# Kernel optimization log

Measured on AMD Instinct MI355X. Metric: run time of the kernel, lower is better.

Reference implementation:

```python
import jax, jax.numpy as jnp
import numpy as np

FA, FB_CAT, FM, HID = 133, 147, 8, 100  # atom feat, bond feat (concat), mol feat, hidden
N_ATOMS, N_BONDS, N_MOLS, MAX_NB = 250000, 500000, 10000, 6
DEPTH = 3


def setup_inputs() -> dict:
    key = jax.random.key(0)
    ks = jax.random.split(key, 10)
    f_atoms = jax.random.normal(ks[0], (N_ATOMS, FA), jnp.float32)
    f_bonds = jax.random.normal(ks[1], (N_BONDS, FB_CAT), jnp.float32)
    f_mol = jax.random.normal(ks[2], (N_MOLS, FM), jnp.float32)
    a2b = jax.random.randint(ks[3], (N_ATOMS, MAX_NB), 0, N_BONDS, jnp.int32)
    b2a = jax.random.randint(ks[4], (N_BONDS,), 0, N_ATOMS, jnp.int32)
    b2revb = jax.random.randint(ks[5], (N_BONDS,), 0, N_BONDS, jnp.int32)
    # contiguous molecules of 25 atoms each -> equivalent of ascope segments
    mol_id = (jnp.arange(N_ATOMS, dtype=jnp.int32) // (N_ATOMS // N_MOLS))
    # parameters (Linear with bias=False): stored as (in, out)
    W_i = jax.random.normal(ks[6], (FB_CAT, HID), jnp.float32) * 0.05
    W_h = jax.random.normal(ks[7], (HID, HID), jnp.float32) * 0.05
    W_o = jax.random.normal(ks[8], (HID + FA, HID), jnp.float32) * 0.05
    return {"f_atoms": f_atoms, "f_bonds": f_bonds, "f_mol": f_mol,
            "W_i": W_i, "W_h": W_h, "W_o": W_o,
            "a2b": a2b, "b2a": b2a, "b2revb": b2revb,
            "mol_id": mol_id, "n_mols": N_MOLS}


def reference(f_atoms, f_bonds, f_mol, W_i, W_h, W_o, a2b, b2a, b2revb, mol_id, n_mols):
    act = jax.nn.relu
    inp = act(f_bonds @ W_i)              # (B, H)
    message = inp
    for _ in range(DEPTH - 1):
        nei = message[a2b]                # (A, MAX_NB, H) gather
        a_message = nei.sum(axis=1)       # (A, H)
        message = a_message[b2a] - message[b2revb]  # (B, H)
        message = act(inp + message @ W_h)
        # dropout p=0 (eval) -> identity
    # readout to atoms
    a_message = message[a2b].sum(axis=1)  # (A, H)
    a_input = jnp.concatenate([f_atoms, a_message], axis=1)  # (A, FA+H)
    atom_hiddens = act(a_input @ W_o)     # (A, H)
    # per-molecule mean over ragged segments (ascope equivalent)
    mol_sum = jax.ops.segment_sum(atom_hiddens, mol_id, num_segments=n_mols)
    counts = jax.ops.segment_sum(jnp.ones((atom_hiddens.shape[0],), atom_hiddens.dtype),
                                 mol_id, num_segments=n_mols)
    mol_vecs = mol_sum / jnp.maximum(counts, 1.0)[:, None]  # zero-vec for empty mols
    mol_vecs = jnp.concatenate([mol_vecs, f_mol], axis=1)   # (M, H+FM)
    return mol_vecs, atom_hiddens
```

## Files before the change

### kernel.cpp

```cpp
#include <hip/hip_runtime.h>

#define THREADS 256
#define MS 128

typedef __bf16 bf16x8 __attribute__((ext_vector_type(8)));
typedef float f32x4 __attribute__((ext_vector_type(4)));
typedef float f32x4u __attribute__((ext_vector_type(4), aligned(4)));

__device__ __forceinline__ unsigned short f2b(float x) {
    unsigned int u = __float_as_uint(x);
    u = (u + 0x7FFFu + ((u >> 16) & 1u)) >> 16;
    return (unsigned short)u;
}
__device__ __forceinline__ float b2f(unsigned short h) {
    return __uint_as_float(((unsigned int)h) << 16);
}
__device__ __forceinline__ bf16x8 as_bf(uint4 q) {
    union { uint4 q; bf16x8 v; } u; u.q = q; return u.v;
}

__device__ __forceinline__ void pack_body(const float* __restrict__ W,
                                          unsigned short* __restrict__ out,
                                          int K, int bid, int l)
{
    int kc = bid / 7, nt = bid - kc * 7;
    int k0 = kc * 32 + (l >> 4) * 8;
    int n = nt * 16 + (l & 15);
    unsigned short v[8];
    #pragma unroll
    for (int j = 0; j < 8; ++j) {
        int k = k0 + j;
        float x = (k < K && n < 100) ? W[(size_t)k * 100 + n] : 0.f;
        v[j] = f2b(x);
    }
    *(uint4*)&out[((size_t)bid * 64 + l) * 8] = *(uint4*)v;
}

__device__ __forceinline__ void pack_wo_body(const float* __restrict__ W,
                                             unsigned short* __restrict__ out,
                                             int bid, int l)
{
    int kc = bid / 7, nt = bid - kc * 7;
    int k0 = kc * 32 + (l >> 4) * 8;
    int n = nt * 16 + (l & 15);
    unsigned short v[8];
    #pragma unroll
    for (int j = 0; j < 8; ++j) {
        int k = k0 + j;
        float x = 0.f;
        if (n < 100) {
            if (k < 100)                  x = W[(size_t)(133 + k) * 100 + n];
            else if (k >= 112 && k < 245) x = W[(size_t)(k - 112) * 100 + n];
        }
        v[j] = f2b(x);
    }
    *(uint4*)&out[((size_t)bid * 64 + l) * 8] = *(uint4*)v;
}

__global__ __launch_bounds__(64) void prep(
    const float* __restrict__ Wi, const float* __restrict__ Wh, const float* __restrict__ Wo,
    unsigned short* __restrict__ wfi, unsigned short* __restrict__ wfh,
    unsigned short* __restrict__ wfo, float* __restrict__ out_mol, int nmol_floats)
{
    int bid = blockIdx.x;
    int l = threadIdx.x;
    if (bid < 35) {
        pack_body(Wi, wfi, 147, bid, l);
    } else if (bid < 63) {
        pack_body(Wh, wfh, 100, bid - 35, l);
    } else if (bid < 119) {
        pack_wo_body(Wo, wfo, bid - 63, l);
    } else {
        int idx = (bid - 119) * 64 + l;
        int stride = (gridDim.x - 119) * 64;
        for (int i = idx; i * 4 < nmol_floats; i += stride)
            *(f32x4*)&out_mol[(size_t)i * 4] = (f32x4){0.f, 0.f, 0.f, 0.f};
    }
}

__global__ __launch_bounds__(THREADS) void gather_sum_bf16(
    const unsigned short* __restrict__ msg, const int* __restrict__ a2b,
    unsigned short* __restrict__ amsg, int A)
{
    int t = blockIdx.x * THREADS + threadIdx.x;
    if (t >= A * 16) return;
    int a = t >> 4;
    int c = t & 15;
    if (c >= 14) {
        *(uint4*)&amsg[(size_t)a * MS + c * 8] = make_uint4(0u, 0u, 0u, 0u);
        return;
    }
    const int* nb = a2b + (size_t)a * 6;
    float s[8];
    #pragma unroll
    for (int e = 0; e < 8; ++e) s[e] = 0.f;
    #pragma unroll
    for (int j = 0; j < 6; ++j) {
        uint4 v = *(const uint4*)&msg[(size_t)nb[j] * MS + c * 8];
        const unsigned short* pv = (const unsigned short*)&v;
        #pragma unroll
        for (int e = 0; e < 8; ++e) s[e] += b2f(pv[e]);
    }
    unsigned short r[8];
    #pragma unroll
    for (int e = 0; e < 8; ++e) r[e] = f2b(s[e]);
    *(uint4*)&amsg[(size_t)a * MS + c * 8] = *(uint4*)r;
}

__global__ __launch_bounds__(THREADS, 2) void gemm_in(
    const float* __restrict__ fb, const unsigned short* __restrict__ wf,
    unsigned short* __restrict__ Y, int M)
{
    constexpr int KS = 168;
    __shared__ char smem[64 * KS * 2];
    unsigned short* Xs = (unsigned short*)smem;
    unsigned short* Os = (unsigned short*)smem;

    const int tid = threadIdx.x;
    const int l = tid & 63, w = tid >> 6;
    const int quad = l >> 4, c15 = l & 15;
    const int row0 = blockIdx.x * 64;

    for (int t = tid; t < 64 * 20; t += THREADS) {
        int rl = t / 20, c = t - rl * 20;
        int rr = min(row0 + rl, M - 1);
        const float* rowp = fb + (size_t)rr * 147 + c * 8;
        unsigned short tt[8];
        if (c < 18) {
            f32x4u x0 = *(const f32x4u*)(rowp);
            f32x4u x1 = *(const f32x4u*)(rowp + 4);
            #pragma unroll
            for (int e = 0; e < 4; ++e) { tt[e] = f2b(x0[e]); tt[4 + e] = f2b(x1[e]); }
        } else if (c == 18) {
            #pragma unroll
            for (int j = 0; j < 8; ++j)
                tt[j] = (j < 3) ? f2b(rowp[j]) : (unsigned short)0;
        } else {
            #pragma unroll
            for (int j = 0; j < 8; ++j) tt[j] = 0;
        }
        *(uint4*)&Xs[(size_t)rl * KS + c * 8] = *(uint4*)tt;
    }
    __syncthreads();

    f32x4 acc[7];
    #pragma unroll
    for (int nt = 0; nt < 7; ++nt) acc[nt] = (f32x4){0.f, 0.f, 0.f, 0.f};
    const unsigned short* xrow = Xs + (size_t)(w * 16 + c15) * KS + quad * 8;
    #pragma unroll
    for (int kc = 0; kc < 5; ++kc) {
        bf16x8 av = *(const bf16x8*)(xrow + kc * 32);
        #pragma unroll
        for (int nt = 0; nt < 7; ++nt) {
            uint4 bq = *(const uint4*)&wf[((size_t)(kc * 7 + nt) * 64 + l) * 8];
            acc[nt] = __builtin_amdgcn_mfma_f32_16x16x32_bf16(av, as_bf(bq), acc[nt], 0, 0, 0);
        }
    }
    __syncthreads();

    #pragma unroll
    for (int nt = 0; nt < 7; ++nt)
        #pragma unroll
        for (int reg = 0; reg < 4; ++reg)
            Os[(w * 16 + quad * 4 + reg) * 136 + nt * 16 + c15] = f2b(fmaxf(acc[nt][reg], 0.f));
    __syncthreads();

    for (int t = tid; t < 64 * 16; t += THREADS) {
        int rl = t >> 4, c = t & 15;
        int rr = row0 + rl;
        if (rr < M) {
            uint4 o = (c < 14) ? *(const uint4*)&Os[rl * 136 + c * 8]
                               : make_uint4(0u, 0u, 0u, 0u);
            *(uint4*)&Y[(size_t)rr * MS + c * 8] = o;
        }
    }
}

__global__ __launch_bounds__(THREADS, 2) void gemm_msg(
    const unsigned short* __restrict__ amsg, const unsigned short* __restrict__ msg,
    const int* __restrict__ b2a, const int* __restrict__ b2revb,
    const unsigned short* __restrict__ wf, const unsigned short* __restrict__ bias,
    unsigned short* __restrict__ Y, int M, int last)
{
    __shared__ unsigned short Os[64 * 136];
    const int tid = threadIdx.x;
    const int l = tid & 63, w = tid >> 6;
    const int quad = l >> 4, c15 = l & 15;
    const int row0 = blockIdx.x * 64;
    const int rc = min(row0 + w * 16 + c15, M - 1);
    const int iA = b2a[rc], iB = b2revb[rc];
    const unsigned short* pa = amsg + (size_t)iA * MS + quad * 8;
    const unsigned short* pb = msg  + (size_t)iB * MS + quad * 8;

    uint4 a1[4], a2[4];
    #pragma unroll
    for (int kc = 0; kc < 4; ++kc) {
        a1[kc] = *(const uint4*)(pa + kc * 32);
        a2[kc] = *(const uint4*)(pb + kc * 32);
    }

    f32x4 acc1[7], acc2[7];
    #pragma unroll
    for (int nt = 0; nt < 7; ++nt) {
        acc1[nt] = (f32x4){0.f, 0.f, 0.f, 0.f};
        acc2[nt] = (f32x4){0.f, 0.f, 0.f, 0.f};
    }
    #pragma unroll
    for (int kc = 0; kc < 4; ++kc) {
        #pragma unroll
        for (int nt = 0; nt < 7; ++nt) {
            uint4 bq = *(const uint4*)&wf[((size_t)(kc * 7 + nt) * 64 + l) * 8];
            acc1[nt] = __builtin_amdgcn_mfma_f32_16x16x32_bf16(as_bf(a1[kc]), as_bf(bq), acc1[nt], 0, 0, 0);
            acc2[nt] = __builtin_amdgcn_mfma_f32_16x16x32_bf16(as_bf(a2[kc]), as_bf(bq), acc2[nt], 0, 0, 0);
        }
    }

    #pragma unroll
    for (int nt = 0; nt < 7; ++nt)
        #pragma unroll
        for (int reg = 0; reg < 4; ++reg)
            Os[(w * 16 + quad * 4 + reg) * 136 + nt * 16 + c15] = f2b(acc1[nt][reg] - acc2[nt][reg]);
    __syncthreads();

    for (int t = tid; t < 64 * 16; t += THREADS) {
        int rl = t >> 4, c = t & 15;
        int rr = row0 + rl;
        if (rr >= M) continue;
        if (c < 14) {
            uint4 o = *(const uint4*)&Os[rl * 136 + c * 8];
            uint4 bq = *(const uint4*)&bias[(size_t)rr * MS + c * 8];
            const unsigned short* po = (const unsigned short*)&o;
            const unsigned short* pq = (const unsigned short*)&bq;
            unsigned short res[8];
            #pragma unroll
            for (int e = 0; e < 8; ++e)
                res[e] = f2b(fmaxf(b2f(po[e]) + b2f(pq[e]), 0.f));
            *(uint4*)&Y[(size_t)rr * MS + c * 8] = *(uint4*)res;
        } else if (!last) {
            *(uint4*)&Y[(size_t)rr * MS + c * 8] = make_uint4(0u, 0u, 0u, 0u);
        }
    }
}

__global__ __launch_bounds__(THREADS, 2) void gemm_out(
    const float* __restrict__ fa, const unsigned short* __restrict__ msg,
    const int* __restrict__ a2b, const unsigned short* __restrict__ wf,
    const int* __restrict__ mol_id, float* __restrict__ Y,
    float* __restrict__ out_mol, int M)
{
    constexpr int XSS = 136;
    __shared__ char smem[64 * 100 * 4];
    __shared__ int mids[64];
    unsigned short* Xs = (unsigned short*)smem;
    float* Os = (float*)smem;

    const int tid = threadIdx.x;
    const int l = tid & 63, w = tid >> 6;
    const int quad = l >> 4, c15 = l & 15;
    const int row0 = blockIdx.x * 64;

    if (tid < 64) {
        int rr = row0 + tid;
        mids[tid] = (rr < M) ? mol_id[rr] : -1;
    }

    uint4 af[5];
    {
        const int r = w * 16 + c15;
        const int rr = min(row0 + r, M - 1);
        const float* fap = fa + (size_t)rr * 133;
        #pragma unroll
        for (int kk = 0; kk < 5; ++kk) {
            int col0 = (kk + 3) * 32 + quad * 8 - 112;
            unsigned short tt[8];
            if (col0 >= 0 && col0 + 7 < 133) {
                f32x4u x0 = *(const f32x4u*)(fap + col0);
                f32x4u x1 = *(const f32x4u*)(fap + col0 + 4);
                #pragma unroll
                for (int e = 0; e < 4; ++e) { tt[e] = f2b(x0[e]); tt[4 + e] = f2b(x1[e]); }
            } else {
                #pragma unroll
                for (int j = 0; j < 8; ++j) {
                    int cc = col0 + j;
                    tt[j] = (cc >= 0 && cc < 133) ? f2b(fap[cc]) : (unsigned short)0;
                }
            }
            af[kk] = *(uint4*)tt;
        }
    }

    for (int t = tid; t < 64 * 16; t += THREADS) {
        int rl = t >> 4, c = t & 15;
        int rr = min(row0 + rl, M - 1);
        uint4 o = make_uint4(0u, 0u, 0u, 0u);
        if (c < 14) {
            const int* nb = a2b + (size_t)rr * 6;
            float s[8];
            #pragma unroll
            for (int e = 0; e < 8; ++e) s[e] = 0.f;
            #pragma unroll
            for (int j = 0; j < 6; ++j) {
                uint4 v = *(const uint4*)&msg[(size_t)nb[j] * MS + c * 8];
                const unsigned short* pv = (const unsigned short*)&v;
                #pragma unroll
                for (int e = 0; e < 8; ++e) s[e] += b2f(pv[e]);
            }
            unsigned short r8[8];
            #pragma unroll
            for (int e = 0; e < 8; ++e) r8[e] = f2b(s[e]);
            o = *(uint4*)r8;
        }
        *(uint4*)&Xs[rl * XSS + c * 8] = o;
    }
    __syncthreads();

    f32x4 acc[7];
    #pragma unroll
    for (int nt = 0; nt < 7; ++nt) acc[nt] = (f32x4){0.f, 0.f, 0.f, 0.f};
    const unsigned short* xrow = Xs + (size_t)(w * 16 + c15) * XSS + quad * 8;
    #pragma unroll
    for (int kc = 0; kc < 8; ++kc) {
        bf16x8 av;
        if (kc < 3)       av = *(const bf16x8*)(xrow + kc * 32);
        else if (kc == 3) av = (quad < 2) ? *(const bf16x8*)(xrow + 3 * 32)
                                          : as_bf(af[0]);
        else              av = as_bf(af[kc - 3]);
        #pragma unroll
        for (int nt = 0; nt < 7; ++nt) {
            uint4 bq = *(const uint4*)&wf[((size_t)(kc * 7 + nt) * 64 + l) * 8];
            acc[nt] = __builtin_amdgcn_mfma_f32_16x16x32_bf16(av, as_bf(bq), acc[nt], 0, 0, 0);
        }
    }
    __syncthreads();

    #pragma unroll
    for (int nt = 0; nt < 7; ++nt) {
        int n = nt * 16 + c15;
        if (n < 100) {
            #pragma unroll
            for (int reg = 0; reg < 4; ++reg)
                Os[(w * 16 + quad * 4 + reg) * 100 + n] = fmaxf(acc[nt][reg], 0.f);
        }
    }
    __syncthreads();

    for (int t = tid; t < 64 * 25; t += THREADS) {
        int rl = t / 25, c = t - rl * 25;
        int rr = row0 + rl;
        if (rr < M)
            *(f32x4*)&Y[(size_t)rr * 100 + c * 4] = *(const f32x4*)&Os[rl * 100 + c * 4];
    }

    if (tid < 100) {
        int c = tid;
        float s = 0.f;
        int cur = mids[0];
        #pragma unroll 1
        for (int rl = 0; rl < 64; ++rl) {
            int mid = mids[rl];
            if (mid != cur) {
                if (cur >= 0) atomicAdd(&out_mol[(size_t)cur * 108 + c], s);
                s = 0.f;
                cur = mid;
            }
            if (mid < 0) break;
            s += Os[rl * 100 + c];
        }
        if (cur >= 0) atomicAdd(&out_mol[(size_t)cur * 108 + c], s);
    }
}

__global__ __launch_bounds__(128) void finalize(
    float* __restrict__ out_mol, const float* __restrict__ f_mol,
    const int* __restrict__ mol_id, int n_atoms)
{
    int m = blockIdx.x;
    int lo = 0, hi = n_atoms;
    while (lo < hi) { int mid = (lo + hi) >> 1; if (mol_id[mid] < m) lo = mid + 1; else hi = mid; }
    int lo2 = lo, hi2 = n_atoms;
    while (lo2 < hi2) { int mid = (lo2 + hi2) >> 1; if (mol_id[mid] < m + 1) lo2 = mid + 1; else hi2 = mid; }
    float inv = 1.0f / fmaxf((float)(lo2 - lo), 1.0f);
    int c = threadIdx.x;
    if (c < 100) {
        out_mol[(size_t)m * 108 + c] *= inv;
    } else if (c < 108) {
        out_mol[(size_t)m * 108 + c] = f_mol[(size_t)m * 8 + (c - 100)];
    }
}

extern "C" void kernel_launch(void* const* d_in, const int* in_sizes, int n_in,
                              void* d_out, int out_size, void* d_ws, size_t ws_size,
                              hipStream_t stream)
{
    const float* f_atoms = (const float*)d_in[0];
    const float* f_bonds = (const float*)d_in[1];
    const float* f_mol   = (const float*)d_in[2];
    const float* W_i     = (const float*)d_in[3];
    const float* W_h     = (const float*)d_in[4];
    const float* W_o     = (const float*)d_in[5];
    const int* a2b    = (const int*)d_in[6];
    const int* b2a    = (const int*)d_in[7];
    const int* b2revb = (const int*)d_in[8];
    const int* mol_id = (const int*)d_in[9];

    const int A    = in_sizes[0] / 133;
    const int B    = in_sizes[1] / 147;
    const int Mmol = in_sizes[2] / 8;

    unsigned short* wsu = (unsigned short*)d_ws;
    unsigned short* wfi  = wsu;
    unsigned short* wfh  = wfi + 35 * 512;
    unsigned short* wfo  = wfh + 28 * 512;
    unsigned short* amsg = wfo + 56 * 512;
    unsigned short* inp  = amsg + (size_t)A * MS;
    unsigned short* msgA = inp  + (size_t)B * MS;
    unsigned short* msgB = msgA + (size_t)B * MS;

    float* out     = (float*)d_out;
    float* out_mol = out;
    float* atom_h  = out + (size_t)Mmol * 108;

    dim3 blk(THREADS);
    int gB = (B + 63) / 64;
    int gA = (A + 63) / 64;
    int gg = (A * 16 + THREADS - 1) / THREADS;

    prep<<<119 + 256, dim3(64), 0, stream>>>(W_i, W_h, W_o, wfi, wfh, wfo,
                                             out_mol, Mmol * 108);

    gemm_in<<<gB, blk, 0, stream>>>(f_bonds, wfi, inp, B);

    gather_sum_bf16<<<gg, blk, 0, stream>>>(inp, a2b, amsg, A);
    gemm_msg<<<gB, blk, 0, stream>>>(amsg, inp, b2a, b2revb, wfh, inp, msgA, B, 0);

    gather_sum_bf16<<<gg, blk, 0, stream>>>(msgA, a2b, amsg, A);
    gemm_msg<<<gB, blk, 0, stream>>>(amsg, msgA, b2a, b2revb, wfh, inp, msgB, B, 1);

    gemm_out<<<gA, blk, 0, stream>>>(f_atoms, msgB, a2b, wfo, mol_id, atom_h, out_mol, A);

    finalize<<<Mmol, dim3(128), 0, stream>>>(out_mol, f_mol, mol_id, A);
}
```

Before: 1.000 ms.

## Fuse all stages into one persistent cooperative kernel with grid syncs

Replaces the sequence of eight separate kernel launches with a single persistent cooperative kernel that loops over tiles for each stage and separates stages with grid-wide barriers. It targets launch overhead and the idle tail between dependent kernels. The old per-stage kernels remain as a fallback if the cooperative launch fails. In exchange, the fused kernel caps occupancy (launch bounds of 4 blocks, grid capped at 8 blocks per CU over 256 CUs), may raise register pressure, and adds grid.sync costs.

```diff
diff --git a/kernel.cpp b/kernel.cpp
--- a/kernel.cpp
+++ b/kernel.cpp
@@ -1,4 +1,6 @@
 #include <hip/hip_runtime.h>
+#include <hip/hip_cooperative_groups.h>
+namespace cg = cooperative_groups;
 
 #define THREADS 256
 #define MS 128
@@ -18,6 +20,7 @@
 __device__ __forceinline__ bf16x8 as_bf(uint4 q) {
     union { uint4 q; bf16x8 v; } u; u.q = q; return u.v;
 }
+
 
 __device__ __forceinline__ void pack_body(const float* __restrict__ W,
                                           unsigned short* __restrict__ out,
@@ -57,33 +60,21 @@
     *(uint4*)&out[((size_t)bid * 64 + l) * 8] = *(uint4*)v;
 }
 
-__global__ __launch_bounds__(64) void prep(
+__device__ __forceinline__ void prep_item(int i,
     const float* __restrict__ Wi, const float* __restrict__ Wh, const float* __restrict__ Wo,
     unsigned short* __restrict__ wfi, unsigned short* __restrict__ wfh,
-    unsigned short* __restrict__ wfo, float* __restrict__ out_mol, int nmol_floats)
-{
-    int bid = blockIdx.x;
-    int l = threadIdx.x;
-    if (bid < 35) {
-        pack_body(Wi, wfi, 147, bid, l);
-    } else if (bid < 63) {
-        pack_body(Wh, wfh, 100, bid - 35, l);
-    } else if (bid < 119) {
-        pack_wo_body(Wo, wfo, bid - 63, l);
-    } else {
-        int idx = (bid - 119) * 64 + l;
-        int stride = (gridDim.x - 119) * 64;
-        for (int i = idx; i * 4 < nmol_floats; i += stride)
-            *(f32x4*)&out_mol[(size_t)i * 4] = (f32x4){0.f, 0.f, 0.f, 0.f};
-    }
-}
-
-__global__ __launch_bounds__(THREADS) void gather_sum_bf16(
+    unsigned short* __restrict__ wfo)
+{
+    int bid = i >> 6, l = i & 63;
+    if (bid < 35)      pack_body(Wi, wfi, 147, bid, l);
+    else if (bid < 63) pack_body(Wh, wfh, 100, bid - 35, l);
+    else               pack_wo_body(Wo, wfo, bid - 63, l);
+}
+
+__device__ __forceinline__ void gather_item(int t,
     const unsigned short* __restrict__ msg, const int* __restrict__ a2b,
-    unsigned short* __restrict__ amsg, int A)
-{
-    int t = blockIdx.x * THREADS + threadIdx.x;
-    if (t >= A * 16) return;
+    unsigned short* __restrict__ amsg)
+{
     int a = t >> 4;
     int c = t & 15;
     if (c >= 14) {
@@ -107,19 +98,15 @@
     *(uint4*)&amsg[(size_t)a * MS + c * 8] = *(uint4*)r;
 }
 
-__global__ __launch_bounds__(THREADS, 2) void gemm_in(
+__device__ __forceinline__ void gemm_in_tile(int row0, int tid,
     const float* __restrict__ fb, const unsigned short* __restrict__ wf,
-    unsigned short* __restrict__ Y, int M)
+    unsigned short* __restrict__ Y, int M, char* smem)
 {
     constexpr int KS = 168;
-    __shared__ char smem[64 * KS * 2];
     unsigned short* Xs = (unsigned short*)smem;
     unsigned short* Os = (unsigned short*)smem;
-
-    const int tid = threadIdx.x;
     const int l = tid & 63, w = tid >> 6;
     const int quad = l >> 4, c15 = l & 15;
-    const int row0 = blockIdx.x * 64;
 
     for (int t = tid; t < 64 * 20; t += THREADS) {
         int rl = t / 20, c = t - rl * 20;
@@ -174,19 +161,18 @@
             *(uint4*)&Y[(size_t)rr * MS + c * 8] = o;
         }
     }
-}
-
-__global__ __launch_bounds__(THREADS, 2) void gemm_msg(
+    __syncthreads();
+}
+
+__device__ __forceinline__ void gemm_msg_tile(int row0, int tid,
     const unsigned short* __restrict__ amsg, const unsigned short* __restrict__ msg,
     const int* __restrict__ b2a, const int* __restrict__ b2revb,
     const unsigned short* __restrict__ wf, const unsigned short* __restrict__ bias,
-    unsigned short* __restrict__ Y, int M, int last)
-{
-    __shared__ unsigned short Os[64 * 136];
-    const int tid = threadIdx.x;
+    unsigned short* __restrict__ Y, int M, int last, char* smem)
+{
+    unsigned short* Os = (unsigned short*)smem;
     const int l = tid & 63, w = tid >> 6;
     const int quad = l >> 4, c15 = l & 15;
-    const int row0 = blockIdx.x * 64;
     const int rc = min(row0 + w * 16 + c15, M - 1);
     const int iA = b2a[rc], iB = b2revb[rc];
     const unsigned short* pa = amsg + (size_t)iA * MS + quad * 8;
@@ -240,24 +226,20 @@
             *(uint4*)&Y[(size_t)rr * MS + c * 8] = make_uint4(0u, 0u, 0u, 0u);
         }
     }
-}
-
-__global__ __launch_bounds__(THREADS, 2) void gemm_out(
+    __syncthreads();
+}
+
+__device__ __forceinline__ void gemm_out_tile(int row0, int tid,
     const float* __restrict__ fa, const unsigned short* __restrict__ msg,
     const int* __restrict__ a2b, const unsigned short* __restrict__ wf,
     const int* __restrict__ mol_id, float* __restrict__ Y,
-    float* __restrict__ out_mol, int M)
+    float* __restrict__ out_mol, int M, char* smem, int* mids)
 {
     constexpr int XSS = 136;
-    __shared__ char smem[64 * 100 * 4];
-    __shared__ int mids[64];
     unsigned short* Xs = (unsigned short*)smem;
     float* Os = (float*)smem;
-
-    const int tid = threadIdx.x;
     const int l = tid & 63, w = tid >> 6;
     const int quad = l >> 4, c15 = l & 15;
-    const int row0 = blockIdx.x * 64;
 
     if (tid < 64) {
         int rr = row0 + tid;
@@ -368,25 +350,140 @@
         }
         if (cur >= 0) atomicAdd(&out_mol[(size_t)cur * 108 + c], s);
     }
-}
-
-__global__ __launch_bounds__(128) void finalize(
+    __syncthreads();
+}
+
+__device__ __forceinline__ void finalize_item(int m, int c,
     float* __restrict__ out_mol, const float* __restrict__ f_mol,
     const int* __restrict__ mol_id, int n_atoms)
 {
-    int m = blockIdx.x;
     int lo = 0, hi = n_atoms;
     while (lo < hi) { int mid = (lo + hi) >> 1; if (mol_id[mid] < m) lo = mid + 1; else hi = mid; }
     int lo2 = lo, hi2 = n_atoms;
     while (lo2 < hi2) { int mid = (lo2 + hi2) >> 1; if (mol_id[mid] < m + 1) lo2 = mid + 1; else hi2 = mid; }
     float inv = 1.0f / fmaxf((float)(lo2 - lo), 1.0f);
-    int c = threadIdx.x;
     if (c < 100) {
         out_mol[(size_t)m * 108 + c] *= inv;
     } else if (c < 108) {
         out_mol[(size_t)m * 108 + c] = f_mol[(size_t)m * 8 + (c - 100)];
     }
 }
+
+
+__global__ __launch_bounds__(THREADS, 4) void fused(
+    const float* __restrict__ fa, const float* __restrict__ fb, const float* __restrict__ fm,
+    const float* __restrict__ Wi, const float* __restrict__ Wh, const float* __restrict__ Wo,
+    const int* __restrict__ a2b, const int* __restrict__ b2a,
+    const int* __restrict__ b2revb, const int* __restrict__ moid,
+    unsigned short* __restrict__ wfi, unsigned short* __restrict__ wfh,
+    unsigned short* __restrict__ wfo, unsigned short* __restrict__ amsg,
+    unsigned short* __restrict__ inp, unsigned short* __restrict__ msgA,
+    unsigned short* __restrict__ msgB,
+    float* __restrict__ atom_h, float* __restrict__ out_mol,
+    int A, int B, int Mmol)
+{
+    __shared__ char smem[25600];
+    __shared__ int mids[64];
+    cg::grid_group grid = cg::this_grid();
+    const int tid = threadIdx.x;
+    const int gt = blockIdx.x * THREADS + tid;
+    const int nth = gridDim.x * THREADS;
+    const int gB = (B + 63) >> 6, gA = (A + 63) >> 6;
+
+    for (int i = gt; i < 119 * 64; i += nth) prep_item(i, Wi, Wh, Wo, wfi, wfh, wfo);
+    for (int i = gt; i * 4 < Mmol * 108; i += nth)
+        *(f32x4*)&out_mol[(size_t)i * 4] = (f32x4){0.f, 0.f, 0.f, 0.f};
+    grid.sync();
+
+    for (int tb = blockIdx.x; tb < gB; tb += gridDim.x)
+        gemm_in_tile(tb * 64, tid, fb, wfi, inp, B, smem);
+    grid.sync();
+
+    for (int t = gt; t < A * 16; t += nth) gather_item(t, inp, a2b, amsg);
+    grid.sync();
+
+    for (int tb = blockIdx.x; tb < gB; tb += gridDim.x)
+        gemm_msg_tile(tb * 64, tid, amsg, inp, b2a, b2revb, wfh, inp, msgA, B, 0, smem);
+    grid.sync();
+
+    for (int t = gt; t < A * 16; t += nth) gather_item(t, msgA, a2b, amsg);
+    grid.sync();
+
+    for (int tb = blockIdx.x; tb < gB; tb += gridDim.x)
+        gemm_msg_tile(tb * 64, tid, amsg, msgA, b2a, b2revb, wfh, inp, msgB, B, 1, smem);
+    grid.sync();
+
+    for (int tb = blockIdx.x; tb < gA; tb += gridDim.x)
+        gemm_out_tile(tb * 64, tid, fa, msgB, a2b, wfo, moid, atom_h, out_mol, A, smem, mids);
+    grid.sync();
+
+    for (int i = gt; i < Mmol * 128; i += nth)
+        finalize_item(i >> 7, i & 127, out_mol, fm, moid, A);
+}
+
+
+__global__ __launch_bounds__(64) void prep(
+    const float* __restrict__ Wi, const float* __restrict__ Wh, const float* __restrict__ Wo,
+    unsigned short* __restrict__ wfi, unsigned short* __restrict__ wfh,
+    unsigned short* __restrict__ wfo, float* __restrict__ out_mol, int nmol_floats)
+{
+    int bid = blockIdx.x;
+    int l = threadIdx.x;
+    if (bid < 119) {
+        prep_item(bid * 64 + l, Wi, Wh, Wo, wfi, wfh, wfo);
+    } else {
+        int idx = (bid - 119) * 64 + l;
+        int stride = (gridDim.x - 119) * 64;
+        for (int i = idx; i * 4 < nmol_floats; i += stride)
+            *(f32x4*)&out_mol[(size_t)i * 4] = (f32x4){0.f, 0.f, 0.f, 0.f};
+    }
+}
+
+__global__ __launch_bounds__(THREADS) void gather_sum_bf16(
+    const unsigned short* __restrict__ msg, const int* __restrict__ a2b,
+    unsigned short* __restrict__ amsg, int A)
+{
+    int t = blockIdx.x * THREADS + threadIdx.x;
+    if (t >= A * 16) return;
+    gather_item(t, msg, a2b, amsg);
+}
+
+__global__ __launch_bounds__(THREADS, 2) void gemm_in(
+    const float* __restrict__ fb, const unsigned short* __restrict__ wf,
+    unsigned short* __restrict__ Y, int M)
+{
+    __shared__ char smem[64 * 168 * 2];
+    gemm_in_tile(blockIdx.x * 64, threadIdx.x, fb, wf, Y, M, smem);
+}
+
+__global__ __launch_bounds__(THREADS, 2) void gemm_msg(
+    const unsigned short* __restrict__ amsg, const unsigned short* __restrict__ msg,
+    const int* __restrict__ b2a, const int* __restrict__ b2revb,
+    const unsigned short* __restrict__ wf, const unsigned short* __restrict__ bias,
+    unsigned short* __restrict__ Y, int M, int last)
+{
+    __shared__ char smem[64 * 136 * 2];
+    gemm_msg_tile(blockIdx.x * 64, threadIdx.x, amsg, msg, b2a, b2revb, wf, bias, Y, M, last, smem);
+}
+
+__global__ __launch_bounds__(THREADS, 2) void gemm_out(
+    const float* __restrict__ fa, const unsigned short* __restrict__ msg,
+    const int* __restrict__ a2b, const unsigned short* __restrict__ wf,
+    const int* __restrict__ mol_id, float* __restrict__ Y,
+    float* __restrict__ out_mol, int M)
+{
+    __shared__ char smem[64 * 100 * 4];
+    __shared__ int mids[64];
+    gemm_out_tile(blockIdx.x * 64, threadIdx.x, fa, msg, a2b, wf, mol_id, Y, out_mol, M, smem, mids);
+}
+
+__global__ __launch_bounds__(128) void finalize(
+    float* __restrict__ out_mol, const float* __restrict__ f_mol,
+    const int* __restrict__ mol_id, int n_atoms)
+{
+    finalize_item(blockIdx.x, threadIdx.x, out_mol, f_mol, mol_id, n_atoms);
+}
+
 
 extern "C" void kernel_launch(void* const* d_in, const int* in_sizes, int n_in,
                               void* d_out, int out_size, void* d_ws, size_t ws_size,
@@ -403,9 +500,9 @@
     const int* b2revb = (const int*)d_in[8];
     const int* mol_id = (const int*)d_in[9];
 
-    const int A    = in_sizes[0] / 133;
-    const int B    = in_sizes[1] / 147;
-    const int Mmol = in_sizes[2] / 8;
+    int A    = in_sizes[0] / 133;
+    int B    = in_sizes[1] / 147;
+    int Mmol = in_sizes[2] / 8;
 
     unsigned short* wsu = (unsigned short*)d_ws;
     unsigned short* wfi  = wsu;
@@ -420,6 +517,30 @@
     float* out_mol = out;
     float* atom_h  = out + (size_t)Mmol * 108;
 
+    static int coop_grid = -2;
+    if (coop_grid == -2) {
+        int nb = 0;
+        hipError_t e = hipOccupancyMaxActiveBlocksPerMultiprocessor(&nb, fused, THREADS, 0);
+        coop_grid = (e == hipSuccess && nb > 0) ? (nb > 8 ? 8 : nb) * 256 : -1;
+    }
+
+    if (coop_grid > 0) {
+        void* args[] = {
+            (void*)&f_atoms, (void*)&f_bonds, (void*)&f_mol,
+            (void*)&W_i, (void*)&W_h, (void*)&W_o,
+            (void*)&a2b, (void*)&b2a, (void*)&b2revb, (void*)&mol_id,
+            (void*)&wfi, (void*)&wfh, (void*)&wfo, (void*)&amsg,
+            (void*)&inp, (void*)&msgA, (void*)&msgB,
+            (void*)&atom_h, (void*)&out_mol,
+            (void*)&A, (void*)&B, (void*)&Mmol
+        };
+        hipError_t rc = hipLaunchCooperativeKernel(fused, dim3(coop_grid), dim3(THREADS),
+                                                   args, 0, stream);
+        if (rc == hipSuccess) return;
+        (void)hipGetLastError();
+        coop_grid = -1;
+    }
+
     dim3 blk(THREADS);
     int gB = (B + 63) / 64;
     int gA = (A + 63) / 64;
@@ -427,16 +548,11 @@
 
     prep<<<119 + 256, dim3(64), 0, stream>>>(W_i, W_h, W_o, wfi, wfh, wfo,
                                              out_mol, Mmol * 108);
-
     gemm_in<<<gB, blk, 0, stream>>>(f_bonds, wfi, inp, B);
-
     gather_sum_bf16<<<gg, blk, 0, stream>>>(inp, a2b, amsg, A);
     gemm_msg<<<gB, blk, 0, stream>>>(amsg, inp, b2a, b2revb, wfh, inp, msgA, B, 0);
-
     gather_sum_bf16<<<gg, blk, 0, stream>>>(msgA, a2b, amsg, A);
     gemm_msg<<<gB, blk, 0, stream>>>(amsg, msgA, b2a, b2revb, wfh, inp, msgB, B, 1);
-
     gemm_out<<<gA, blk, 0, stream>>>(f_atoms, msgB, a2b, wfo, mol_id, atom_h, out_mol, A);
-
     finalize<<<Mmol, dim3(128), 0, stream>>>(out_mol, f_mol, mol_id, A);
 }
```

Result: slower. 1.978 ms (+97.7%).
